# Performance work log

Measured on AMD Instinct MI355X. Metric: run time of the kernel, lower is better.

Reference implementation:

```python
import jax, jax.numpy as jnp
import numpy as np

DECAY = 0.99


def setup_inputs() -> dict:
    key = jax.random.key(0)
    k1, k2, k3 = jax.random.split(key, 3)
    B, L, D, N = 8, 2048, 512, 1024
    x = jax.random.normal(k1, (B, L, D), dtype=jnp.float32)
    codebook = jax.random.normal(k2, (N, D), dtype=jnp.float32)
    ema_weight = jax.random.normal(k3, (N, D), dtype=jnp.float32)
    counts = jnp.ones((N,), dtype=jnp.float32)
    return {"x": x, "codebook": codebook, "ema_weight": ema_weight, "counts": counts}


def reference(x, codebook, ema_weight, counts):
    # x: [B, L, D]; codebook/ema_weight: [N, D]; counts: [N]
    n_tokens = codebook.shape[0]
    # avoids materializing the [B,L,N,D] difference tensor of the naive form)
    x_sq = jnp.sum(x * x, axis=-1, keepdims=True)            # [B, L, 1]
    c_sq = jnp.sum(codebook * codebook, axis=-1)             # [N]
    xc = jnp.einsum('bld,nd->bln', x, codebook)              # [B, L, N]
    distances = jnp.sqrt(jnp.maximum(x_sq - 2.0 * xc + c_sq, 0.0))
    indices = jnp.argmin(distances, axis=-1)                 # [B, L]
    encodings = jax.nn.one_hot(indices, n_tokens, dtype=jnp.float32)  # [B, L, N]
    # train=True branch: EMA codebook update
    counts_new = DECAY * counts + (1.0 - DECAY) * jnp.sum(encodings, axis=(0, 1))
    dw = jnp.einsum('bln,bld->nd', encodings, x)             # [N, D]
    ema_new = DECAY * ema_weight + (1.0 - DECAY) * dw
    codebook_new = ema_new / counts_new[:, None]
    # quantization with straight-through estimator
    quantized = jnp.einsum('bln,nd->bld', encodings, codebook_new)  # [B, L, D]
    quantized = x + jax.lax.stop_gradient(quantized - x)
    # optax.l2_loss(x, quantized) = 0.5 * (x - quantized)^2
    codebook_loss = jnp.mean(0.5 * jnp.square(x - quantized))
    return quantized, codebook_loss, indices
```

## Files before the change

kernel.cpp:

```cpp
#include <hip/hip_runtime.h>
#include <hip/hip_bf16.h>

constexpr int Dd   = 512;
constexpr int Nn   = 1024;
constexpr int Ttok = 16384;
constexpr float DECAYc = 0.99f;
constexpr float GAP = 3.0f;
constexpr int CH = 16;

typedef short bf16x8 __attribute__((ext_vector_type(8)));
typedef float f32x4  __attribute__((ext_vector_type(4)));

__device__ inline unsigned cvtpk(float lo, float hi) {
  unsigned r;
  asm("v_cvt_pk_bf16_f32 %0, %1, %2" : "=v"(r) : "v"(lo), "v"(hi));
  return r;
}

constexpr int NB_CB = 256, NB_Z = 32, NB_X = 2048;
constexpr int ZF4 = 131328;
__global__ __launch_bounds__(256) void k_prep(
    const float* __restrict__ cb, const float* __restrict__ x,
    unsigned short* __restrict__ cbh, float* __restrict__ csq,
    unsigned short* __restrict__ xh, float4* __restrict__ zbase,
    float* __restrict__ sxxp) {
  const int b = blockIdx.x, tid = threadIdx.x;
  if (b < NB_CB) {
    const int n = b * 4 + (tid >> 6), l = tid & 63;
    const float4* r = (const float4*)(cb + (size_t)n * Dd);
    float4 a = r[l], c = r[l + 64];
    float ss = a.x*a.x + a.y*a.y + a.z*a.z + a.w*a.w
             + c.x*c.x + c.y*c.y + c.z*c.z + c.w*c.w;
    uint2 ua, uc;
    ua.x = cvtpk(a.x, a.y); ua.y = cvtpk(a.z, a.w);
    uc.x = cvtpk(c.x, c.y); uc.y = cvtpk(c.z, c.w);
    ((uint2*)(cbh + (size_t)n * Dd))[l]      = ua;
    ((uint2*)(cbh + (size_t)n * Dd))[l + 64] = uc;
#pragma unroll
    for (int o = 32; o; o >>= 1) ss += __shfl_down(ss, o);
    if (l == 0) csq[n] = ss;
  } else if (b < NB_CB + NB_Z) {
    const float4 z = make_float4(0.f, 0.f, 0.f, 0.f);
    for (int i = (b - NB_CB) * 256 + tid; i < ZF4; i += NB_Z * 256)
      zbase[i] = z;
  } else {
    const int bx = b - (NB_CB + NB_Z);
    float sx = 0.f;
#pragma unroll
    for (int k = 0; k < 2; ++k) {
      const int i = bx * 512 + k * 256 + tid;
      float4 a = ((const float4*)x)[i * 2];
      float4 c = ((const float4*)x)[i * 2 + 1];
      sx += a.x*a.x + a.y*a.y + a.z*a.z + a.w*a.w
          + c.x*c.x + c.y*c.y + c.z*c.z + c.w*c.w;
      uint4 o;
      o.x = cvtpk(a.x, a.y); o.y = cvtpk(a.z, a.w);
      o.z = cvtpk(c.x, c.y); o.w = cvtpk(c.z, c.w);
      ((uint4*)xh)[i] = o;
    }
#pragma unroll
    for (int o = 32; o; o >>= 1) sx += __shfl_down(sx, o);
    if ((tid & 63) == 0) sxxp[bx * 4 + (tid >> 6)] = sx;
  }
}

__global__ __launch_bounds__(256) void k_gemm_scores(
    const unsigned short* __restrict__ cbh, const unsigned short* __restrict__ xh,
    const float* __restrict__ csq, float4* __restrict__ part) {
  __shared__ unsigned short As[2][128 * 32];
  __shared__ unsigned short Bs[2][128 * 32];
  const int tid = threadIdx.x;
  const int w = tid >> 6, l = tid & 63;
  const int b = blockIdx.x;
  const int s = (b & 7) * 128 + (b >> 3);
  const int cm = s & 7;
  const int tn = s >> 3;
  const int wr = w >> 1, wc = w & 1;

  const int srow = tid >> 2;
  const int scol = (tid & 3) * 8;

  f32x4 acc[4][4] = {};

  const unsigned short* gA0 = cbh + (size_t)(cm * 128) * Dd;
  const unsigned short* gB0 = xh  + (size_t)(tn * 128) * Dd;

#define ISSUE(KC, BUF) do {                                                   \
    const int k0_ = (KC) * 32;                                                \
    _Pragma("unroll")                                                         \
    for (int p = 0; p < 2; ++p) {                                             \
      const unsigned short* ga = gA0 + (size_t)(p * 64 + srow) * Dd + k0_ + scol; \
      const unsigned short* gb = gB0 + (size_t)(p * 64 + srow) * Dd + k0_ + scol; \
      char* la = (char*)&As[BUF][0] + p * 4096 + w * 1024;                    \
      char* lb = (char*)&Bs[BUF][0] + p * 4096 + w * 1024;                    \
      __builtin_amdgcn_global_load_lds((const __attribute__((address_space(1))) void*)ga, \
                                       (__attribute__((address_space(3))) void*)la, 16, 0, 0); \
      __builtin_amdgcn_global_load_lds((const __attribute__((address_space(1))) void*)gb, \
                                       (__attribute__((address_space(3))) void*)lb, 16, 0, 0); \
    }                                                                         \
  } while (0)

  ISSUE(0, 0);

  for (int kc = 0; kc < Dd / 32; ++kc) {
    __syncthreads();
    if (kc + 1 < Dd / 32) ISSUE(kc + 1, (kc + 1) & 1);
    const unsigned short* Ab = &As[kc & 1][0];
    const unsigned short* Bb = &Bs[kc & 1][0];
    const int ra = l & 15;
    const int kb = (l >> 4) * 8;
    bf16x8 af[4], bfr[4];
#pragma unroll
    for (int m = 0; m < 4; ++m)
      af[m] = *(const bf16x8*)&Ab[(wr * 64 + m * 16 + ra) * 32 + kb];
#pragma unroll
    for (int n = 0; n < 4; ++n)
      bfr[n] = *(const bf16x8*)&Bb[(wc * 64 + n * 16 + ra) * 32 + kb];
#pragma unroll
    for (int m = 0; m < 4; ++m)
#pragma unroll
      for (int n = 0; n < 4; ++n)
        acc[m][n] = __builtin_amdgcn_mfma_f32_16x16x32_bf16(af[m], bfr[n], acc[m][n], 0, 0, 0);
  }
#undef ISSUE

  const int base4 = wr * 64 + (l >> 4) * 4;
  float4 cs[4];
#pragma unroll
  for (int m = 0; m < 4; ++m)
    cs[m] = *(const float4*)&csq[cm * 128 + base4 + m * 16];

  const int slot = cm * 2 + wr;
  const int tok0 = tn * 128 + wc * 64 + (l & 15);

#pragma unroll
  for (int n = 0; n < 4; ++n) {
    float v0 = 3.4e38f, v1 = 3.4e38f, v2 = 3.4e38f;
    int i0 = 0x7fffffff, i1 = 0x7fffffff;
#pragma unroll
    for (int m = 0; m < 4; ++m) {
#pragma unroll
      for (int r = 0; r < 4; ++r) {
        float sv = fmaf(-2.0f, acc[m][n][r], ((const float*)&cs[m])[r]);
        int idx = cm * 128 + base4 + m * 16 + r;
        if (sv < v0)      { v2 = v1; v1 = v0; i1 = i0; v0 = sv; i0 = idx; }
        else if (sv < v1) { v2 = v1; v1 = sv; i1 = idx; }
        else if (sv < v2) { v2 = sv; }
      }
    }
#pragma unroll
    for (int o = 16; o <= 32; o <<= 1) {
      float w0 = __shfl_xor(v0, o), w1 = __shfl_xor(v1, o), w2 = __shfl_xor(v2, o);
      int  j0 = __shfl_xor(i0, o), j1 = __shfl_xor(i1, o);
      bool f = (w0 < v0) || (w0 == v0 && j0 < i0);
      float A0 = f ? w0 : v0, A1 = f ? w1 : v1, A2 = f ? w2 : v2;
      int  Ai0 = f ? j0 : i0, Ai1 = f ? j1 : i1;
      float B0 = f ? v0 : w0, B1 = f ? v1 : w1;
      int  Bi0 = f ? i0 : j0;
      bool g = (A1 < B0) || (A1 == B0 && Ai1 < Bi0);
      v0 = A0; i0 = Ai0;
      v1 = g ? A1 : B0; i1 = g ? Ai1 : Bi0;
      v2 = g ? fminf(A2, B0) : fminf(A1, B1);
    }
    if ((l >> 4) == 0)
      part[(size_t)slot * Ttok + tok0 + n * 16] = make_float4(
          v0, v1, __uint_as_float((unsigned)i0 | ((unsigned)i1 << 16)), v2);
  }
}

__device__ inline void rescore(int n, const float4& xa, const float4& xb,
                               const float* __restrict__ cb,
                               const float* __restrict__ csq, int l,
                               float& bestv, int& besti) {
  const float4* cr = (const float4*)(cb + (size_t)n * Dd);
  float4 ca = cr[l * 2], cc = cr[l * 2 + 1];
  float p = xa.x*ca.x + xa.y*ca.y + xa.z*ca.z + xa.w*ca.w
          + xb.x*cc.x + xb.y*cc.y + xb.z*cc.z + xb.w*cc.w;
#pragma unroll
  for (int o = 32; o; o >>= 1) p += __shfl_xor(p, o);
  float sc = csq[n] - 2.0f * p;
  if (sc < bestv || (sc == bestv && n < besti)) { bestv = sc; besti = n; }
}

__device__ inline void rescore_half(int h, const float* __restrict__ xrow,
                                    const float* __restrict__ cb,
                                    const float* __restrict__ csq, int l,
                                    float& bestv, int& besti) {
  int n = h * 64 + l;
  const float4* cr = (const float4*)(cb + (size_t)n * Dd);
  const float4* xr = (const float4*)xrow;
  float p = 0.f;
#pragma unroll 8
  for (int j = 0; j < 128; ++j) {
    float4 c4 = cr[j], x4 = xr[j];
    p += c4.x*x4.x + c4.y*x4.y + c4.z*x4.z + c4.w*x4.w;
  }
  float sc = csq[n] - 2.0f * p;
#pragma unroll
  for (int o = 1; o < 64; o <<= 1) {
    float ov = __shfl_xor(sc, o); int oi = __shfl_xor(n, o);
    if (ov < sc || (ov == sc && oi < n)) { sc = ov; n = oi; }
  }
  if (sc < bestv || (sc == bestv && n < besti)) { bestv = sc; besti = n; }
}

__global__ __launch_bounds__(256) void k_select(
    const float4* __restrict__ part, const float* __restrict__ x,
    const float* __restrict__ cb, const float* __restrict__ csq,
    int* __restrict__ idxb, float* __restrict__ idxf, float* __restrict__ hist) {
  const int tid = threadIdx.x, wid = tid >> 6, l = tid & 63;
  const int t = blockIdx.x * 4 + wid;
  float v0 = 3.4e38f, v1 = 3.4e38f, v2 = 3.4e38f;
  int i0 = 0x7fffffff, i1 = 0x7fffffff;
  if (l < 16) {
    float4 e = part[(size_t)l * Ttok + t];
    v0 = e.x; v1 = e.y; v2 = e.w;
    unsigned ii = __float_as_uint(e.z);
    i0 = (int)(ii & 0xffff); i1 = (int)(ii >> 16);
  }
  float A0 = v0, A1 = v1; int Ai0 = i0, Ai1 = i1;
#pragma unroll
  for (int o = 1; o < 16; o <<= 1) {
    float w0 = __shfl_xor(A0, o), w1 = __shfl_xor(A1, o);
    int  j0 = __shfl_xor(Ai0, o), j1 = __shfl_xor(Ai1, o);
    bool f = (w0 < A0) || (w0 == A0 && j0 < Ai0);
    float B0 = f ? A0 : w0; int Bi0 = f ? Ai0 : j0;
    float W1 = f ? w1 : A1; int Wi1 = f ? j1 : Ai1;
    if (f) { A0 = w0; Ai0 = j0; }
    bool g = (B0 < W1) || (B0 == W1 && Bi0 < Wi1);
    A1 = g ? B0 : W1; Ai1 = g ? Bi0 : Wi1;
  }
  const float m  = __shfl(A0, 0);
  const float g1 = __shfl(A1, 0);
  const int   gi = __shfl(Ai0, 0);
  int besti;
  if (g1 - m > GAP) {
    besti = gi;
  } else {
    const float thr = m + GAP;
    const float* xrow = x + (size_t)t * Dd;
    const float4* xr = (const float4*)xrow;
    float4 xa = xr[l * 2], xb = xr[l * 2 + 1];
    float bestv = 3.4e38f; besti = 0x7fffffff;
    for (int h = 0; h < 16; ++h) {
      float b0 = __shfl(v0, h);
      if (b0 > thr) continue;
      float b1 = __shfl(v1, h), b2 = __shfl(v2, h);
      int bi0 = __shfl(i0, h), bi1 = __shfl(i1, h);
      if (b2 <= thr) {
        rescore_half(h, xrow, cb, csq, l, bestv, besti);
      } else {
        rescore(bi0, xa, xb, cb, csq, l, bestv, besti);
        if (b1 <= thr) rescore(bi1, xa, xb, cb, csq, l, bestv, besti);
      }
    }
  }
  if (l == 0) {
    idxb[t] = besti;
    idxf[t] = (float)besti;
    atomicAdd(&hist[besti], 1.0f);
  }
}

__global__ __launch_bounds__(256) void k_offsets(const float* __restrict__ hist,
                                                 int* __restrict__ cursor) {
  __shared__ int wsum[4];
  const int tid = threadIdx.x, l = tid & 63, wd = tid >> 6;
  const int base = tid * 4;
  int c0 = (int)hist[base], c1 = (int)hist[base + 1],
      c2 = (int)hist[base + 2], c3 = (int)hist[base + 3];
  int sum = c0 + c1 + c2 + c3;
  int sc = sum;
#pragma unroll
  for (int o = 1; o < 64; o <<= 1) { int v = __shfl_up(sc, o); if (l >= o) sc += v; }
  if (l == 63) wsum[wd] = sc;
  __syncthreads();
  int wbase = 0;
  for (int i = 0; i < wd; ++i) wbase += wsum[i];
  int e = wbase + sc - sum;
  cursor[base]     = e;
  cursor[base + 1] = e + c0;
  cursor[base + 2] = e + c0 + c1;
  cursor[base + 3] = e + c0 + c1 + c2;
}

__global__ __launch_bounds__(256) void k_scatter(const int* __restrict__ idxb,
                                                 int* __restrict__ cursor,
                                                 int* __restrict__ bucket,
                                                 int* __restrict__ bcode) {
  int t = blockIdx.x * 256 + threadIdx.x;
  if (t < Ttok) {
    int n = idxb[t];
    int p = atomicAdd(&cursor[n], 1);
    bucket[p] = t;
    bcode[p] = n;
  }
}

__global__ __launch_bounds__(512) void k_dw_part(
    const float* __restrict__ x, const int* __restrict__ bucket,
    const int* __restrict__ bcode, float* __restrict__ dw) {
  __shared__ int sh_t[CH], sh_n[CH];
  const int tid = threadIdx.x;
  const int p0 = blockIdx.x * CH;
  if (tid < CH) { sh_t[tid] = bucket[p0 + tid]; sh_n[tid] = bcode[p0 + tid]; }
  __syncthreads();
  float v[CH];
#pragma unroll
  for (int j = 0; j < CH; ++j)
    v[j] = x[(size_t)sh_t[j] * Dd + tid];
  float acc = v[0]; int cur = sh_n[0];
#pragma unroll
  for (int j = 1; j < CH; ++j) {
    int n = sh_n[j];
    if (n != cur) { atomicAdd(&dw[(size_t)cur * Dd + tid], acc); acc = 0.f; cur = n; }
    acc += v[j];
  }
  atomicAdd(&dw[(size_t)cur * Dd + tid], acc);
}

__global__ __launch_bounds__(128) void k_lossterms(
    const float* __restrict__ ema, const float* __restrict__ dw,
    const float* __restrict__ counts, const float* __restrict__ hist,
    float* __restrict__ sxqp, float* __restrict__ sqqp) {
  const int n = blockIdx.x, tid = threadIdx.x;
  const float hc = hist[n];
  const float inv = 1.0f / (DECAYc * counts[n] + (1.0f - DECAYc) * hc);
  f32x4 e = ((const f32x4*)(ema + (size_t)n * Dd))[tid];
  f32x4 d = ((const f32x4*)(dw  + (size_t)n * Dd))[tid];
  f32x4 q = (DECAYc * e + (1.0f - DECAYc) * d) * inv;
  float xq = q[0]*d[0] + q[1]*d[1] + q[2]*d[2] + q[3]*d[3];
  float qq = q[0]*q[0] + q[1]*q[1] + q[2]*q[2] + q[3]*q[3];
#pragma unroll
  for (int o = 32; o; o >>= 1) { xq += __shfl_down(xq, o); qq += __shfl_down(qq, o); }
  __shared__ float sx[2], sq[2];
  const int wd = tid >> 6, l = tid & 63;
  if (l == 0) { sx[wd] = xq; sq[wd] = qq; }
  __syncthreads();
  if (tid == 0) { sxqp[n] = sx[0] + sx[1]; sqqp[n] = hc * (sq[0] + sq[1]); }
}

__global__ __launch_bounds__(256) void quant_out(
    const float* __restrict__ ema, const float* __restrict__ dw,
    const float* __restrict__ counts, const float* __restrict__ hist,
    const int* __restrict__ idx, float* __restrict__ out_q) {
  const int e0 = blockIdx.x * 256 + threadIdx.x;
  const int gsz = 524288;
  int n[4];
#pragma unroll
  for (int j = 0; j < 4; ++j) n[j] = idx[(e0 + j * gsz) >> 7];
  float inv[4];
#pragma unroll
  for (int j = 0; j < 4; ++j)
    inv[j] = 1.0f / (DECAYc * counts[n[j]] + (1.0f - DECAYc) * hist[n[j]]);
  f32x4 e4[4], d4[4];
#pragma unroll
  for (int j = 0; j < 4; ++j) {
    const int e = e0 + j * gsz;
    e4[j] = ((const f32x4*)(ema + (size_t)n[j] * Dd))[e & 127];
    d4[j] = ((const f32x4*)(dw  + (size_t)n[j] * Dd))[e & 127];
  }
#pragma unroll
  for (int j = 0; j < 4; ++j) {
    f32x4 q = (DECAYc * e4[j] + (1.0f - DECAYc) * d4[j]) * inv[j];
    __builtin_nontemporal_store(q, &((f32x4*)out_q)[e0 + j * gsz]);
  }
}

__global__ __launch_bounds__(256) void loss_final(
    const float* __restrict__ sxxp, const float* __restrict__ sxqp,
    const float* __restrict__ sqqp, float* __restrict__ out_loss) {
  const int tid = threadIdx.x;
  double acc = 0.0;
  for (int i = tid; i < 8192; i += 256) acc += (double)sxxp[i];
  for (int i = tid; i < 1024; i += 256) acc -= 2.0 * (double)sxqp[i];
  for (int i = tid; i < 1024; i += 256) acc += (double)sqqp[i];
#pragma unroll
  for (int o = 32; o; o >>= 1) acc += __shfl_down(acc, o);
  __shared__ double red[4];
  const int wd = tid >> 6, l = tid & 63;
  if (l == 0) red[wd] = acc;
  __syncthreads();
  if (tid == 0)
    *out_loss = (float)((red[0] + red[1] + red[2] + red[3]) *
                        (0.5 / ((double)Ttok * (double)Dd)));
}

extern "C" void kernel_launch(void* const* d_in, const int* in_sizes, int n_in,
                              void* d_out, int out_size, void* d_ws, size_t ws_size,
                              hipStream_t stream) {
  const float* x      = (const float*)d_in[0];
  const float* cb     = (const float*)d_in[1];
  const float* ema    = (const float*)d_in[2];
  const float* counts = (const float*)d_in[3];

  float* out      = (float*)d_out;
  float* q_out    = out;
  float* loss_out = out + (size_t)Ttok * Dd;
  float* idxf_out = loss_out + 1;
  float4* part = (float4*)q_out;
  unsigned short* xh = (unsigned short*)(q_out + 2097152);

  float* ws = (float*)d_ws;
  unsigned short* cbh = (unsigned short*)ws;
  float* dw      = ws + 262144;
  float* hist    = ws + 786432;
  float* csq     = ws + 787460;
  int*   cursor  = (int*)(ws + 789508);
  int*   bucket  = (int*)(ws + 790532);
  int*   bcode   = (int*)(ws + 806916);
  int*   idxb    = (int*)(ws + 823300);
  float* sxxp    = ws + 839684;
  float* sxqp    = ws + 847876;
  float* sqqp    = ws + 848900;

  k_prep<<<NB_CB + NB_Z + NB_X, 256, 0, stream>>>(cb, x, cbh, csq, xh,
                                                  (float4*)dw, sxxp);
  k_gemm_scores<<<(Nn / 128) * (Ttok / 128), 256, 0, stream>>>(cbh, xh, csq, part);
  k_select<<<Ttok / 4, 256, 0, stream>>>(part, x, cb, csq, idxb, idxf_out, hist);
  k_offsets<<<1, 256, 0, stream>>>(hist, cursor);
  k_scatter<<<Ttok / 256, 256, 0, stream>>>(idxb, cursor, bucket, bcode);
  k_dw_part<<<Ttok / CH, 512, 0, stream>>>(x, bucket, bcode, dw);
  k_lossterms<<<Nn, 128, 0, stream>>>(ema, dw, counts, hist, sxqp, sqqp);
  quant_out<<<2048, 256, 0, stream>>>(ema, dw, counts, hist, idxb, q_out);
  loss_final<<<1, 256, 0, stream>>>(sxxp, sxqp, sqqp, loss_out);
}
```

Before: 118.0 us.

## Triple-buffer GEMM LDS loads and fold loss-term kernel into quant_out

The scores GEMM moves from double to triple buffering in LDS. It keeps two k-chunks in flight and uses an explicit vmcnt wait plus s_barrier instead of __syncthreads, with the k-loop fully unrolled, so global-to-LDS latency is hidden better. Separately, the per-codebook loss-term kernel is merged into quant_out as extra blocks, which removes one kernel launch. In exchange the GEMM uses more LDS, which may lower occupancy, and the hand-written waitcnt depends on the exact count of outstanding loads.

```diff
diff --git a/kernel.cpp b/kernel.cpp
--- a/kernel.cpp
+++ b/kernel.cpp
@@ -67,8 +67,8 @@
 __global__ __launch_bounds__(256) void k_gemm_scores(
     const unsigned short* __restrict__ cbh, const unsigned short* __restrict__ xh,
     const float* __restrict__ csq, float4* __restrict__ part) {
-  __shared__ unsigned short As[2][128 * 32];
-  __shared__ unsigned short Bs[2][128 * 32];
+  __shared__ unsigned short As[3][128 * 32];
+  __shared__ unsigned short Bs[3][128 * 32];
   const int tid = threadIdx.x;
   const int w = tid >> 6, l = tid & 63;
   const int b = blockIdx.x;
@@ -101,12 +101,18 @@
   } while (0)
 
   ISSUE(0, 0);
-
+  ISSUE(1, 1);
+
+#pragma unroll
   for (int kc = 0; kc < Dd / 32; ++kc) {
-    __syncthreads();
-    if (kc + 1 < Dd / 32) ISSUE(kc + 1, (kc + 1) & 1);
-    const unsigned short* Ab = &As[kc & 1][0];
-    const unsigned short* Bb = &Bs[kc & 1][0];
+    if (kc < Dd / 32 - 1)
+      asm volatile("s_waitcnt vmcnt(4)\n\ts_barrier" ::: "memory");
+    else
+      asm volatile("s_waitcnt vmcnt(0)\n\ts_barrier" ::: "memory");
+    __builtin_amdgcn_sched_barrier(0);
+    if (kc + 2 < Dd / 32) ISSUE(kc + 2, (kc + 2) % 3);
+    const unsigned short* Ab = &As[kc % 3][0];
+    const unsigned short* Bb = &Bs[kc % 3][0];
     const int ra = l & 15;
     const int kb = (l >> 4) * 8;
     bf16x8 af[4], bfr[4];
@@ -319,32 +325,33 @@
   atomicAdd(&dw[(size_t)cur * Dd + tid], acc);
 }
 
-__global__ __launch_bounds__(128) void k_lossterms(
-    const float* __restrict__ ema, const float* __restrict__ dw,
-    const float* __restrict__ counts, const float* __restrict__ hist,
-    float* __restrict__ sxqp, float* __restrict__ sqqp) {
-  const int n = blockIdx.x, tid = threadIdx.x;
-  const float hc = hist[n];
-  const float inv = 1.0f / (DECAYc * counts[n] + (1.0f - DECAYc) * hc);
-  f32x4 e = ((const f32x4*)(ema + (size_t)n * Dd))[tid];
-  f32x4 d = ((const f32x4*)(dw  + (size_t)n * Dd))[tid];
-  f32x4 q = (DECAYc * e + (1.0f - DECAYc) * d) * inv;
-  float xq = q[0]*d[0] + q[1]*d[1] + q[2]*d[2] + q[3]*d[3];
-  float qq = q[0]*q[0] + q[1]*q[1] + q[2]*q[2] + q[3]*q[3];
-#pragma unroll
-  for (int o = 32; o; o >>= 1) { xq += __shfl_down(xq, o); qq += __shfl_down(qq, o); }
-  __shared__ float sx[2], sq[2];
-  const int wd = tid >> 6, l = tid & 63;
-  if (l == 0) { sx[wd] = xq; sq[wd] = qq; }
-  __syncthreads();
-  if (tid == 0) { sxqp[n] = sx[0] + sx[1]; sqqp[n] = hc * (sq[0] + sq[1]); }
-}
-
 __global__ __launch_bounds__(256) void quant_out(
     const float* __restrict__ ema, const float* __restrict__ dw,
     const float* __restrict__ counts, const float* __restrict__ hist,
-    const int* __restrict__ idx, float* __restrict__ out_q) {
-  const int e0 = blockIdx.x * 256 + threadIdx.x;
+    const int* __restrict__ idx, float* __restrict__ out_q,
+    float* __restrict__ sxqp, float* __restrict__ sqqp) {
+  const int b = blockIdx.x, tid = threadIdx.x;
+  if (b >= 2048) {
+    const int n = b - 2048;
+    if (tid < 128) {
+      const float hc = hist[n];
+      const float inv = 1.0f / (DECAYc * counts[n] + (1.0f - DECAYc) * hc);
+      f32x4 e = ((const f32x4*)(ema + (size_t)n * Dd))[tid];
+      f32x4 d = ((const f32x4*)(dw  + (size_t)n * Dd))[tid];
+      f32x4 q = (DECAYc * e + (1.0f - DECAYc) * d) * inv;
+      float xq = q[0]*d[0] + q[1]*d[1] + q[2]*d[2] + q[3]*d[3];
+      float qq = q[0]*q[0] + q[1]*q[1] + q[2]*q[2] + q[3]*q[3];
+#pragma unroll
+      for (int o = 32; o; o >>= 1) { xq += __shfl_down(xq, o); qq += __shfl_down(qq, o); }
+      __shared__ float sx[2], sq[2];
+      const int wd = tid >> 6, l = tid & 63;
+      if (l == 0) { sx[wd] = xq; sq[wd] = qq; }
+      __syncthreads();
+      if (tid == 0) { sxqp[n] = sx[0] + sx[1]; sqqp[n] = hc * (sq[0] + sq[1]); }
+    }
+    return;
+  }
+  const int e0 = b * 256 + tid;
   const int gsz = 524288;
   int n[4];
 #pragma unroll
@@ -421,7 +428,7 @@
   k_offsets<<<1, 256, 0, stream>>>(hist, cursor);
   k_scatter<<<Ttok / 256, 256, 0, stream>>>(idxb, cursor, bucket, bcode);
   k_dw_part<<<Ttok / CH, 512, 0, stream>>>(x, bucket, bcode, dw);
-  k_lossterms<<<Nn, 128, 0, stream>>>(ema, dw, counts, hist, sxqp, sqqp);
-  quant_out<<<2048, 256, 0, stream>>>(ema, dw, counts, hist, idxb, q_out);
+  quant_out<<<3072, 256, 0, stream>>>(ema, dw, counts, hist, idxb, q_out,
+                                      sxqp, sqqp);
   loss_final<<<1, 256, 0, stream>>>(sxxp, sxqp, sqqp, loss_out);
 }
```

After: 114.1 us. 3.3% less time.
